# Performance work log

Measured on AMD Instinct MI355X. Metric: run time of the kernel, lower is better.

The kernel has to match this reference:

```python
import jax, jax.numpy as jnp
import numpy as np

B, N, D = 4, 2048, 512
H = 8
DH = D // H
FF = 2 * D


def setup_inputs() -> dict:
    key = jax.random.key(0)
    ks = jax.random.split(key, 16)
    s = lambda fan_in: 1.0 / np.sqrt(fan_in)
    inp = {
        "x0": jax.random.normal(ks[0], (B, N, D), jnp.float32),
        "x1": jax.random.normal(ks[1], (B, N, D), jnp.float32),
        # projections (torch Linear: weight [out, in])
        "Wqk": jax.random.uniform(ks[2], (D, D), jnp.float32, -s(D), s(D)),
        "bqk": jax.random.uniform(ks[3], (D,), jnp.float32, -s(D), s(D)),
        "Wv": jax.random.uniform(ks[4], (D, D), jnp.float32, -s(D), s(D)),
        "bv": jax.random.uniform(ks[5], (D,), jnp.float32, -s(D), s(D)),
        "Wo": jax.random.uniform(ks[6], (D, D), jnp.float32, -s(D), s(D)),
        "bo": jax.random.uniform(ks[7], (D,), jnp.float32, -s(D), s(D)),
        # FFN: Linear(2D,2D) -> LayerNorm(2D) -> GELU -> Linear(2D,D)
        "Wf1": jax.random.uniform(ks[8], (FF, FF), jnp.float32, -s(FF), s(FF)),
        "bf1": jax.random.uniform(ks[9], (FF,), jnp.float32, -s(FF), s(FF)),
        "ln_g": jnp.ones((FF,), jnp.float32),
        "ln_b": jnp.zeros((FF,), jnp.float32),
        "Wf2": jax.random.uniform(ks[10], (D, FF), jnp.float32, -s(FF), s(FF)),
        "bf2": jax.random.uniform(ks[11], (D,), jnp.float32, -s(FF), s(FF)),
    }
    return inp


def _split_heads(t):
    # [B,N,D] -> [B,H,N,DH]
    return t.reshape(B, N, H, DH).transpose(0, 2, 1, 3)


def _attn(q, k, v):
    # q,k,v: [B,H,N,DH]; scale by sqrt(d_k) as in the torch Attention module
    scores = jnp.einsum("bhnd,bhmd->bhnm", q, k) / jnp.sqrt(jnp.float32(DH))
    attn = jax.nn.softmax(scores, axis=-1)
    return jnp.einsum("bhnm,bhmd->bhnd", attn, v)


def _merge_heads(t):
    # [B,H,N,DH] -> [B,N,D]
    return t.transpose(0, 2, 1, 3).reshape(B, N, D)


def _ffn(x, Wf1, bf1, ln_g, ln_b, Wf2, bf2):
    h = x @ Wf1.T + bf1
    mu = jnp.mean(h, axis=-1, keepdims=True)
    var = jnp.mean(jnp.square(h - mu), axis=-1, keepdims=True)
    h = (h - mu) / jnp.sqrt(var + 1e-5) * ln_g + ln_b
    h = jax.nn.gelu(h, approximate=False)
    return h @ Wf2.T + bf2


def reference(x0, x1, Wqk, bqk, Wv, bv, Wo, bo, Wf1, bf1, ln_g, ln_b, Wf2, bf2):
    qk0 = _split_heads(x0 @ Wqk.T + bqk)
    qk1 = _split_heads(x1 @ Wqk.T + bqk)
    v0 = _split_heads(x0 @ Wv.T + bv)
    v1 = _split_heads(x1 @ Wv.T + bv)

    m0 = _merge_heads(_attn(qk0, qk1, v1)) @ Wo.T + bo
    m1 = _merge_heads(_attn(qk1, qk0, v0)) @ Wo.T + bo

    y0 = x0 + _ffn(jnp.concatenate([x0, m0], -1), Wf1, bf1, ln_g, ln_b, Wf2, bf2)
    y1 = x1 + _ffn(jnp.concatenate([x1, m1], -1), Wf1, bf1, ln_g, ln_b, Wf2, bf2)
    return (y0, y1)
```

## Files before the change

kernel.cpp:

```cpp
#include <hip/hip_runtime.h>
#include <hip/hip_bf16.h>
#include <math.h>

typedef __bf16 bf16;
typedef __bf16 bf16x8 __attribute__((ext_vector_type(8)));
typedef __bf16 bf16x4 __attribute__((ext_vector_type(4)));
typedef float  f32x4  __attribute__((ext_vector_type(4)));
typedef float  f32x16 __attribute__((ext_vector_type(16)));
typedef unsigned int u32x2 __attribute__((ext_vector_type(2)));

#define DEVI __device__ __forceinline__

DEVI void async16(bf16* lds, const bf16* g) {
    __builtin_amdgcn_global_load_lds(
        (const __attribute__((address_space(1))) unsigned int*)g,
        (__attribute__((address_space(3))) unsigned int*)lds, 16, 0, 0);
}
DEVI f32x4 mfma16(bf16x8 a, bf16x8 b, f32x4 c) {
    return __builtin_amdgcn_mfma_f32_16x16x32_bf16(a, b, c, 0, 0, 0);
}
DEVI f32x16 mfma32(bf16x8 a, bf16x8 b, f32x16 c) {
    return __builtin_amdgcn_mfma_f32_32x32x16_bf16(a, b, c, 0, 0, 0);
}
DEVI unsigned cvtpk(float lo, float hi) {
    unsigned r;
    asm("v_cvt_pk_bf16_f32 %0, %1, %2" : "=v"(r) : "v"(lo), "v"(hi));
    return r;
}
DEVI void pl32(unsigned &a, unsigned &b) {
    u32x2 r = __builtin_amdgcn_permlane32_swap(a, b, false, false);
    a = r.x; b = r.y;
}
DEVI bf16x8 mk8(unsigned a0, unsigned a1, unsigned b0, unsigned b1) {
    union { unsigned u[4]; bf16x8 v; } U;
    U.u[0] = a0; U.u[1] = a1; U.u[2] = b0; U.u[3] = b1;
    return U.v;
}

__global__ __launch_bounds__(256) void prep(
    const float* __restrict__ x0, const float* __restrict__ x1, bf16* __restrict__ Xbf,
    const float* __restrict__ Wqk, const float* __restrict__ Wv,
    const float* __restrict__ Wf1, const float* __restrict__ Wf2,
    bf16* __restrict__ Wqkv, bf16* __restrict__ Wbig, bf16* __restrict__ Wf1Rb,
    bf16* __restrict__ Wf2b,
    const float* __restrict__ Wo, bf16* __restrict__ WoT,
    const float* __restrict__ bo, const float* __restrict__ bf1,
    float* __restrict__ bf1p)
{
    __shared__ float Ls[64][65];
    const int bid = blockIdx.x, t = threadIdx.x;
    if (bid < 8192) {
        long i = (long)bid * 256 + t;
        long r = i >> 7, c = (i & 127) * 4;
        const float* src = (r < 8192) ? (x0 + r * 512 + c) : (x1 + (r - 8192) * 512 + c);
        float4 v = *(const float4*)src;
        bf16x4 o;
        o[0] = (bf16)v.x; o[1] = (bf16)v.y; o[2] = (bf16)v.z; o[3] = (bf16)v.w;
        *(bf16x4*)(Xbf + r * 1024 + c) = o;
    } else if (bid < 10240) {
        long i = (long)(bid - 8192) * 256 + t;
        const float* s; bf16* d;
        if (i < 131072) {
            s = (i < 65536) ? Wqk + i * 4 : Wv + (i - 65536) * 4;
            d = Wqkv + i * 4;
        } else if (i < 393216) {
            long e = (i - 131072) * 4, r = e >> 10, c = e & 1023;
            s = Wf1 + e;
            d = (c < 512) ? (Wbig + r * 1024 + c) : (Wf1Rb + r * 512 + (c - 512));
        } else {
            s = Wf2 + (i - 393216) * 4;
            d = Wf2b + (i - 393216) * 4;
        }
        float4 v = *(const float4*)s;
        bf16x4 o;
        o[0] = (bf16)v.x; o[1] = (bf16)v.y; o[2] = (bf16)v.z; o[3] = (bf16)v.w;
        *(bf16x4*)d = o;
    } else if (bid < 10304) {
        const int bb = bid - 10240;
        const int bi = bb & 7, bj = bb >> 3;
        const int i0 = bi * 64, j0 = bj * 64;
        const int r0 = t >> 4, c4 = (t & 15) * 4;
#pragma unroll
        for (int it = 0; it < 4; it++) {
            int row = r0 + 16 * it;
            float4 v = *(const float4*)(Wo + (long)(i0 + row) * 512 + j0 + c4);
            Ls[row][c4] = v.x; Ls[row][c4 + 1] = v.y;
            Ls[row][c4 + 2] = v.z; Ls[row][c4 + 3] = v.w;
        }
        __syncthreads();
#pragma unroll
        for (int it = 0; it < 4; it++) {
            int orow = r0 + 16 * it;
            bf16x4 o;
#pragma unroll
            for (int k = 0; k < 4; k++) o[k] = (bf16)Ls[c4 + k][orow];
            *(bf16x4*)(WoT + (long)(j0 + orow) * 512 + i0 + c4) = o;
        }
    } else {
        const int w = t >> 6, lane = t & 63;
        const int row = (bid - 10304) * 4 + w;
        const float* rp = Wf1 + (long)row * 1024 + 512 + lane * 8;
        float4 a = *(const float4*)rp;
        float4 b = *(const float4*)(rp + 4);
        const float* bp = bo + lane * 8;
        float4 c = *(const float4*)bp;
        float4 d = *(const float4*)(bp + 4);
        float s = a.x * c.x + a.y * c.y + a.z * c.z + a.w * c.w +
                  b.x * d.x + b.y * d.y + b.z * d.z + b.w * d.w;
#pragma unroll
        for (int k = 1; k < 64; k <<= 1) s += __shfl_xor(s, k);
        if (lane == 0) bf1p[row] = bf1[row] + s;
    }
}

template <int MODE>
__global__ __launch_bounds__(256) void gemm_bt(
    const bf16* __restrict__ A, long lda,
    const bf16* __restrict__ B, long ldb,
    const float* __restrict__ bias,
    void* __restrict__ Cout, long ldc,
    const float* __restrict__ res0, const float* __restrict__ res1,
    const float* __restrict__ bias2, void* __restrict__ Cout2,
    int M, int N, int K, float scale)
{
    __shared__ bf16 As[128 * 64];
    __shared__ bf16 Bs[128 * 64];
    const int t = threadIdx.x;
    const int w = t >> 6, lane = t & 63, quad = lane >> 4, m15 = lane & 15;
    const int wm = w >> 1, wn = w & 1;
    const int nbx = N >> 7;
    const int xcd = blockIdx.x & 7, local = blockIdx.x >> 3;
    const int mtiles_per_xcd = (int)(gridDim.x >> 3) / nbx;
    const int by = xcd * mtiles_per_xcd + local / nbx;
    const int bx = local % nbx;
    const long m0 = (long)by * 128, n0 = (long)bx * 128;

    f32x4 acc[4][4] = {};

    for (int k0 = 0; k0 < K; k0 += 64) {
#pragma unroll
        for (int i = 0; i < 4; i++) {
            int idx = i * 256 + t, row = idx >> 3, p = idx & 7;
            int gc = k0 + ((p ^ (row & 7)) * 8);
            async16(As + idx * 8, A + (m0 + row) * lda + gc);
            async16(Bs + idx * 8, B + (n0 + row) * ldb + gc);
        }
        __syncthreads();
#pragma unroll
        for (int kk = 0; kk < 2; kk++) {
            bf16x8 af[4], bfr[4];
#pragma unroll
            for (int mt = 0; mt < 4; mt++) {
                int row = wm * 64 + mt * 16 + m15;
                af[mt] = *(const bf16x8*)(As + row * 64 + (((kk * 4 + quad) ^ (row & 7)) * 8));
            }
#pragma unroll
            for (int nt = 0; nt < 4; nt++) {
                int row = wn * 64 + nt * 16 + m15;
                bfr[nt] = *(const bf16x8*)(Bs + row * 64 + (((kk * 4 + quad) ^ (row & 7)) * 8));
            }
#pragma unroll
            for (int mt = 0; mt < 4; mt++)
#pragma unroll
                for (int nt = 0; nt < 4; nt++)
                    acc[mt][nt] = mfma16(af[mt], bfr[nt], acc[mt][nt]);
        }
        __syncthreads();
    }

#pragma unroll
    for (int nt = 0; nt < 4; nt++) {
        long col = n0 + wn * 64 + nt * 16 + m15;
#pragma unroll
        for (int mt = 0; mt < 4; mt++) {
            long row = m0 + wm * 64 + mt * 16 + quad * 4;
            if (MODE == 0) {
                bf16* C = (bf16*)Cout;
                float bs = bias[col];
#pragma unroll
                for (int r = 0; r < 4; r++)
                    C[(row + r) * ldc + col] = (bf16)(acc[mt][nt][r] + bs);
            } else if (MODE == 4) {
                bf16* C = (bf16*)Cout;
#pragma unroll
                for (int r = 0; r < 4; r++)
                    C[(row + r) * ldc + col] = (bf16)acc[mt][nt][r];
            } else {
                float* C = (float*)Cout;
                float bs = bias[col];
#pragma unroll
                for (int r = 0; r < 4; r++) {
                    long grow = row + r;
                    const float* rs = (grow < 8192) ? (res0 + grow * 512)
                                                    : (res1 + (grow - 8192) * 512);
                    C[grow * ldc + col] = acc[mt][nt][r] + bs + rs[col];
                }
            }
        }
    }
}

template <int MODE>
__global__ __launch_bounds__(512, 2) void pipe_gemm(
    const bf16* __restrict__ A, long lda,
    const bf16* __restrict__ B, long ldb,
    const float* __restrict__ bias,
    void* __restrict__ Cout, long ldc,
    const float* __restrict__ bias2, void* __restrict__ Cout2,
    int M, int N, int K, float scale)
{
    __shared__ bf16 lds[65536];
    bf16* As = lds;
    bf16* Bs = lds + 32768;

    const int t = threadIdx.x;
    const int w = t >> 6, lane = t & 63, quad = lane >> 4, m15 = lane & 15;
    const int wm = w >> 2, wn = w & 3;
    const int nbx = N >> 8;
    const int xcd = blockIdx.x & 7, local = blockIdx.x >> 3;
    const int mtiles_per_xcd = (int)(gridDim.x >> 3) / nbx;
    const int by = xcd * mtiles_per_xcd + local / nbx;
    const int bx = local % nbx;
    const long m0 = (long)by * 256, n0 = (long)bx * 256;
    const int nt = K >> 6;

    f32x4 acc[8][4] = {};

    auto stage = [&](int kt) {
        const int slot = kt & 1;
        bf16* Ad = As + slot * 16384;
        bf16* Bd = Bs + slot * 16384;
        const int k0 = kt * 64;
#pragma unroll
        for (int i = 0; i < 4; i++) {
            int idx = i * 512 + t, row = idx >> 3, p = idx & 7;
            int gc = k0 + ((p ^ (row & 7)) * 8);
            async16(Ad + idx * 8, A + (m0 + row) * lda + gc);
        }
#pragma unroll
        for (int i = 0; i < 4; i++) {
            int idx = i * 512 + t, row = idx >> 3, p = idx & 7;
            int gc = k0 + ((p ^ (row & 7)) * 8);
            async16(Bd + idx * 8, B + (n0 + row) * ldb + gc);
        }
    };

    stage(0);
    stage(1);

    for (int kt = 0; kt < nt; kt++) {
        if (kt + 1 < nt) {
            asm volatile("s_waitcnt vmcnt(8)" ::: "memory");
        } else {
            asm volatile("s_waitcnt vmcnt(0)" ::: "memory");
        }
        __builtin_amdgcn_s_barrier();
        __builtin_amdgcn_sched_barrier(0);

        const bf16* Asl = As + (kt & 1) * 16384;
        const bf16* Bsl = Bs + (kt & 1) * 16384;
#pragma unroll
        for (int ksub = 0; ksub < 2; ksub++) {
            bf16x8 af[8], bfr[4];
#pragma unroll
            for (int mf = 0; mf < 8; mf++) {
                int row = wm * 128 + mf * 16 + m15;
                af[mf] = *(const bf16x8*)(Asl + row * 64 + (((ksub * 4 + quad) ^ (row & 7)) * 8));
            }
#pragma unroll
            for (int nf = 0; nf < 4; nf++) {
                int row = wn * 64 + nf * 16 + m15;
                bfr[nf] = *(const bf16x8*)(Bsl + row * 64 + (((ksub * 4 + quad) ^ (row & 7)) * 8));
            }
            __builtin_amdgcn_s_setprio(1);
#pragma unroll
            for (int mf = 0; mf < 8; mf++)
#pragma unroll
                for (int nf = 0; nf < 4; nf++)
                    acc[mf][nf] = mfma16(af[mf], bfr[nf], acc[mf][nf]);
            __builtin_amdgcn_s_setprio(0);
        }

        __builtin_amdgcn_sched_barrier(0);
        __builtin_amdgcn_s_barrier();
        __builtin_amdgcn_sched_barrier(0);
        if (kt + 2 < nt) stage(kt + 2);
    }

#pragma unroll
    for (int nf = 0; nf < 4; nf++) {
        long col = n0 + wn * 64 + nf * 16 + m15;
#pragma unroll
        for (int mf = 0; mf < 8; mf++) {
            long row = m0 + wm * 128 + mf * 16 + quad * 4;
            if (MODE == 0) {
                bf16* C = (bf16*)Cout;
                float bs = bias[col];
#pragma unroll
                for (int r = 0; r < 4; r++)
                    C[(row + r) * ldc + col] = (bf16)(acc[mf][nf][r] + bs);
            } else {
                if (col < 512) {
                    bf16* C = (bf16*)Cout;
                    float bs = bias[col];
#pragma unroll
                    for (int r = 0; r < 4; r++)
                        C[(row + r) * ldc + col] = (bf16)((acc[mf][nf][r] + bs) * scale);
                } else {
                    bf16* V = (bf16*)Cout2;
                    long v = col - 512;
                    float bs = bias2[v];
                    bf16x4 pv;
#pragma unroll
                    for (int r = 0; r < 4; r++) pv[r] = (bf16)(acc[mf][nf][r] + bs);
                    *(bf16x4*)(V + v * 16384 + row) = pv;
                }
            }
        }
    }
}

__global__ __launch_bounds__(256, 4) void flash_attn(const bf16* __restrict__ QK,
                                                     const bf16* __restrict__ VT,
                                                     bf16* __restrict__ o)
{
    __shared__ bf16 lds[16384];

    const int t = threadIdx.x, w = t >> 6, lane = t & 63;
    const int l31 = lane & 31, hi = lane >> 5;
    const int j = blockIdx.x;
    const int hs = j & 63;
    const int qt = j >> 6;
    const int h = hs & 7, b = (hs >> 3) & 3, dir = hs >> 5;
    const long qrow0  = (long)dir * 8192 + b * 2048 + qt * 128;
    const long kvrow0 = (long)(1 - dir) * 8192 + b * 2048;
    const int hc = h * 64;

#pragma unroll
    for (int i = 0; i < 4; i++) {
        int idx = i * 256 + t, row = idx >> 3, p = idx & 7;
        async16(lds + idx * 8, QK + (qrow0 + row) * 512 + hc + ((p ^ (row & 7)) * 8));
    }
    __syncthreads();
    bf16x8 qf[4];
    {
        int qrow = w * 32 + l31;
#pragma unroll
        for (int kd = 0; kd < 4; kd++)
            qf[kd] = *(const bf16x8*)(lds + qrow * 64 + (((kd * 2 + hi) ^ (qrow & 7)) * 8));
    }
    __syncthreads();

#pragma unroll
    for (int i = 0; i < 2; i++) {
        int idx = i * 256 + t, row = idx >> 3, p = idx & 7;
        async16(lds + idx * 8, QK + (kvrow0 + row) * 512 + hc + ((p ^ (row & 7)) * 8));
    }
#pragma unroll
    for (int i = 0; i < 2; i++) {
        int idx = i * 256 + t, row = idx >> 3, p = idx & 7;
        async16(lds + 8192 + idx * 8, VT + (long)(hc + row) * 16384 + kvrow0 + ((p ^ (row & 7)) * 8));
    }

    f32x16 oacc[2] = {};
    f32x16 racc = {};
    bf16x8 ones;
#pragma unroll
    for (int k = 0; k < 8; k++) ones[k] = (bf16)1.0f;

    for (int kb = 0; kb < 32; kb++) {
        bf16* Kc = lds + (kb & 1) * 4096;
        bf16* Vc = lds + 8192 + (kb & 1) * 4096;

        asm volatile("s_waitcnt vmcnt(0)" ::: "memory");
        __builtin_amdgcn_s_barrier();

        if (kb < 31) {
            const long knext = kvrow0 + (kb + 1) * 64;
            bf16* Kn = lds + ((kb + 1) & 1) * 4096;
            bf16* Vn = lds + 8192 + ((kb + 1) & 1) * 4096;
#pragma unroll
            for (int i = 0; i < 2; i++) {
                int idx = i * 256 + t, row = idx >> 3, p = idx & 7;
                async16(Kn + idx * 8, QK + (knext + row) * 512 + hc + ((p ^ (row & 7)) * 8));
            }
#pragma unroll
            for (int i = 0; i < 2; i++) {
                int idx = i * 256 + t, row = idx >> 3, p = idx & 7;
                async16(Vn + idx * 8, VT + (long)(hc + row) * 16384 + knext + ((p ^ (row & 7)) * 8));
            }
        }

#pragma unroll
        for (int kb2 = 0; kb2 < 2; kb2++) {
            const int krow = kb2 * 32 + l31;
            const int ksw = krow & 7;
            bf16x8 kf0 = *(const bf16x8*)(Kc + krow * 64 + (((0 + hi) ^ ksw) * 8));
            bf16x8 kf1 = *(const bf16x8*)(Kc + krow * 64 + (((2 + hi) ^ ksw) * 8));
            bf16x8 kf2 = *(const bf16x8*)(Kc + krow * 64 + (((4 + hi) ^ ksw) * 8));
            bf16x8 kf3 = *(const bf16x8*)(Kc + krow * 64 + (((6 + hi) ^ ksw) * 8));

            f32x16 s0 = {};
            __builtin_amdgcn_s_setprio(1);
            s0 = mfma32(kf0, qf[0], s0);
            s0 = mfma32(kf1, qf[1], s0);
            s0 = mfma32(kf2, qf[2], s0);
            s0 = mfma32(kf3, qf[3], s0);
            __builtin_amdgcn_s_setprio(0);

#pragma unroll
            for (int r = 0; r < 16; r++) s0[r] = exp2f(s0[r]);

#pragma unroll
            for (int sh = 0; sh < 2; sh++) {
                const int ks = kb2 * 2 + sh;
                unsigned a00 = cvtpk(s0[8 * sh + 0], s0[8 * sh + 1]);
                unsigned a01 = cvtpk(s0[8 * sh + 2], s0[8 * sh + 3]);
                unsigned b00 = cvtpk(s0[8 * sh + 4], s0[8 * sh + 5]);
                unsigned b01 = cvtpk(s0[8 * sh + 6], s0[8 * sh + 7]);
                pl32(a00, b00); pl32(a01, b01);
                bf16x8 pa0 = mk8(a00, a01, b00, b01);

                __builtin_amdgcn_s_setprio(1);
#pragma unroll
                for (int db = 0; db < 2; db++) {
                    const int vrow = db * 32 + l31;
                    bf16x8 vf = *(const bf16x8*)(Vc + vrow * 64 + (((ks * 2 + hi) ^ (vrow & 7)) * 8));
                    oacc[db] = mfma32(pa0, vf, oacc[db]);
                }
                racc = mfma32(pa0, ones, racc);
                __builtin_amdgcn_s_setprio(0);
            }
        }
    }

#pragma unroll
    for (int reg = 0; reg < 16; reg++) {
        const int q = (reg & 3) + 8 * (reg >> 2) + 4 * hi;
        const float inv = 1.f / racc[reg];
        const long row = qrow0 + w * 32 + q;
#pragma unroll
        for (int db = 0; db < 2; db++)
            o[row * 1024 + hc + db * 32 + l31] = (bf16)(oacc[db][reg] * inv);
    }
}

__global__ __launch_bounds__(256) void ln_gelu(bf16* __restrict__ H,
                                               const float* __restrict__ g,
                                               const float* __restrict__ bta)
{
    const int row = blockIdx.x, t = threadIdx.x;
    const int w = t >> 6, lane = t & 63;
    bf16* hp = H + (long)row * 1024 + t * 4;
    bf16x4 hv = *(const bf16x4*)hp;
    float h[4];
#pragma unroll
    for (int j = 0; j < 4; j++) h[j] = (float)hv[j];
    float s1 = h[0] + h[1] + h[2] + h[3];
    float s2 = h[0] * h[0] + h[1] * h[1] + h[2] * h[2] + h[3] * h[3];
#pragma unroll
    for (int d = 1; d < 64; d <<= 1) {
        s1 += __shfl_xor(s1, d);
        s2 += __shfl_xor(s2, d);
    }
    __shared__ float rbuf[8];
    if (lane == 0) { rbuf[w] = s1; rbuf[4 + w] = s2; }
    __syncthreads();
    s1 = rbuf[0] + rbuf[1] + rbuf[2] + rbuf[3];
    s2 = rbuf[4] + rbuf[5] + rbuf[6] + rbuf[7];
    const float mu = s1 * (1.f / 1024.f);
    const float var = s2 * (1.f / 1024.f) - mu * mu;
    const float rstd = rsqrtf(var + 1e-5f);
    bf16x4 out;
#pragma unroll
    for (int j = 0; j < 4; j++) {
        int c = t * 4 + j;
        float x = (h[j] - mu) * rstd * g[c] + bta[c];
        float y = 0.5f * x * (1.f + erff(x * 0.70710678118654752f));
        out[j] = (bf16)y;
    }
    *(bf16x4*)hp = out;
}

extern "C" void kernel_launch(void* const* d_in, const int* in_sizes, int n_in,
                              void* d_out, int out_size, void* d_ws, size_t ws_size,
                              hipStream_t stream)
{
    const float* x0  = (const float*)d_in[0];
    const float* x1  = (const float*)d_in[1];
    const float* Wqk = (const float*)d_in[2];
    const float* bqk = (const float*)d_in[3];
    const float* Wv  = (const float*)d_in[4];
    const float* bv  = (const float*)d_in[5];
    const float* Wo  = (const float*)d_in[6];
    const float* bo  = (const float*)d_in[7];
    const float* Wf1 = (const float*)d_in[8];
    const float* bf1 = (const float*)d_in[9];
    const float* lng = (const float*)d_in[10];
    const float* lnb = (const float*)d_in[11];
    const float* Wf2 = (const float*)d_in[12];
    const float* bf2 = (const float*)d_in[13];

    char* ws = (char*)d_ws;
    bf16* Xbf   = (bf16*)ws; ws += 16384L * 1024 * 2;
    bf16* QKbf  = (bf16*)ws;
    bf16* Hbuf  = (bf16*)ws;
    ws += 16384L * 512 * 2;
    bf16* VtG   = (bf16*)ws; ws += 16384L * 512 * 2;
    bf16* Wqkv  = (bf16*)ws; ws += 1024L * 512 * 2;
    bf16* Wbig  = (bf16*)ws; ws += 1024L * 1024 * 2;
    bf16* Wf1Rb = (bf16*)ws; ws += 1024L * 512 * 2;
    bf16* Wf2b  = (bf16*)ws; ws += 512L * 1024 * 2;
    bf16* WoT   = (bf16*)ws; ws += 512L * 512 * 2;
    float* bf1p = (float*)ws; ws += 1024 * 4;

    const float qs = 0.42466090014400953f;

    prep<<<10560, 256, 0, stream>>>(x0, x1, Xbf, Wqk, Wv, Wf1, Wf2,
                                    Wqkv, Wbig, Wf1Rb, Wf2b, Wo, WoT, bo, bf1, bf1p);

    gemm_bt<4><<<32, 256, 0, stream>>>(Wf1Rb, 512, WoT, 512, nullptr,
                                       Wbig + 512, 1024, nullptr, nullptr,
                                       nullptr, nullptr, 1024, 512, 512, 1.f);

    pipe_gemm<5><<<256, 512, 0, stream>>>(Xbf, 1024, Wqkv, 512, bqk,
                                          QKbf, 512, bv, VtG,
                                          16384, 1024, 512, qs);

    flash_attn<<<1024, 256, 0, stream>>>(QKbf, VtG, Xbf + 512);

    pipe_gemm<0><<<256, 512, 0, stream>>>(Xbf, 1024, Wbig, 1024, bf1p,
                                          Hbuf, 1024, nullptr, nullptr,
                                          16384, 1024, 1024, 1.f);
    ln_gelu<<<16384, 256, 0, stream>>>(Hbuf, lng, lnb);
    gemm_bt<1><<<512, 256, 0, stream>>>(Hbuf, 1024, Wf2b, 1024, bf2,
                                        d_out, 512, x0, x1,
                                        nullptr, nullptr, 16384, 512, 1024, 1.f);
}
```

Measured before the change: 353.3 us.

## Software-pipeline attention softmax/PV across key blocks and add pipelined FFN2 GEMM

The flash attention loop is restructured so the second half's softmax and PV step for one key block runs during the next block's QK MFMAs. V gets a triple-buffered LDS ring so the previous block's V stays valid while the next one loads. The final FFN projection moves from gemm_bt to a new 512-thread double-buffered GEMM with XCD-aware tile mapping and fused bias and residual. This adds LDS use and register pressure (an extra score accumulator) in exchange for better MFMA/VALU overlap.

Result: slower. 360.7 us (+2.1%).

```diff
diff --git a/kernel.cpp b/kernel.cpp
--- a/kernel.cpp
+++ b/kernel.cpp
@@ -320,11 +320,117 @@
     }
 }
 
+__global__ __launch_bounds__(512, 2) void pipe_ffn2(
+    const bf16* __restrict__ A, long lda,
+    const bf16* __restrict__ B, long ldb,
+    const float* __restrict__ bias,
+    float* __restrict__ C, long ldc,
+    const float* __restrict__ res0, const float* __restrict__ res1,
+    int M, int N, int K)
+{
+    __shared__ bf16 lds[49152];
+    bf16* As = lds;
+    bf16* Bs = lds + 16384;
+
+    const int t = threadIdx.x;
+    const int w = t >> 6, lane = t & 63, quad = lane >> 4, m15 = lane & 15;
+    const int wm = w >> 2, wn = w & 3;
+    const int nbx = N >> 8;
+    const int xcd = blockIdx.x & 7, local = blockIdx.x >> 3;
+    const int mtiles_per_xcd = (int)(gridDim.x >> 3) / nbx;
+    const int by = xcd * mtiles_per_xcd + local / nbx;
+    const int bx = local % nbx;
+    const long m0 = (long)by * 128, n0 = (long)bx * 256;
+    const int nt = K >> 6;
+
+    f32x4 acc[4][4] = {};
+
+    auto stage = [&](int kt) {
+        const int slot = kt & 1;
+        bf16* Ad = As + slot * 8192;
+        bf16* Bd = Bs + slot * 16384;
+        const int k0 = kt * 64;
+#pragma unroll
+        for (int i = 0; i < 2; i++) {
+            int idx = i * 512 + t, row = idx >> 3, p = idx & 7;
+            int gc = k0 + ((p ^ (row & 7)) * 8);
+            async16(Ad + idx * 8, A + (m0 + row) * lda + gc);
+        }
+#pragma unroll
+        for (int i = 0; i < 4; i++) {
+            int idx = i * 512 + t, row = idx >> 3, p = idx & 7;
+            int gc = k0 + ((p ^ (row & 7)) * 8);
+            async16(Bd + idx * 8, B + (n0 + row) * ldb + gc);
+        }
+    };
+
+    stage(0);
+    stage(1);
+
+    for (int kt = 0; kt < nt; kt++) {
+        if (kt + 1 < nt) {
+            asm volatile("s_waitcnt vmcnt(6)" ::: "memory");
+        } else {
+            asm volatile("s_waitcnt vmcnt(0)" ::: "memory");
+        }
+        __builtin_amdgcn_s_barrier();
+        __builtin_amdgcn_sched_barrier(0);
+
+        const bf16* Asl = As + (kt & 1) * 8192;
+        const bf16* Bsl = Bs + (kt & 1) * 16384;
+#pragma unroll
+        for (int ksub = 0; ksub < 2; ksub++) {
+            bf16x8 af[4], bfr[4];
+#pragma unroll
+            for (int mf = 0; mf < 4; mf++) {
+                int row = wm * 64 + mf * 16 + m15;
+                af[mf] = *(const bf16x8*)(Asl + row * 64 + (((ksub * 4 + quad) ^ (row & 7)) * 8));
+            }
+#pragma unroll
+            for (int nf = 0; nf < 4; nf++) {
+                int row = wn * 64 + nf * 16 + m15;
+                bfr[nf] = *(const bf16x8*)(Bsl + row * 64 + (((ksub * 4 + quad) ^ (row & 7)) * 8));
+            }
+            __builtin_amdgcn_s_setprio(1);
+#pragma unroll
+            for (int mf = 0; mf < 4; mf++)
+#pragma unroll
+                for (int nf = 0; nf < 4; nf++)
+                    acc[mf][nf] = mfma16(af[mf], bfr[nf], acc[mf][nf]);
+            __builtin_amdgcn_s_setprio(0);
+        }
+
+        __builtin_amdgcn_sched_barrier(0);
+        __builtin_amdgcn_s_barrier();
+        __builtin_amdgcn_sched_barrier(0);
+        if (kt + 2 < nt) stage(kt + 2);
+    }
+
+#pragma unroll
+    for (int nf = 0; nf < 4; nf++) {
+        long col = n0 + wn * 64 + nf * 16 + m15;
+        float bs = bias[col];
+#pragma unroll
+        for (int mf = 0; mf < 4; mf++) {
+            long row = m0 + wm * 64 + mf * 16 + quad * 4;
+#pragma unroll
+            for (int r = 0; r < 4; r++) {
+                long grow = row + r;
+                const float* rs = (grow < 8192) ? (res0 + grow * 512)
+                                                : (res1 + (grow - 8192) * 512);
+                C[grow * ldc + col] = acc[mf][nf][r] + bs + rs[col];
+            }
+        }
+    }
+}
+
 __global__ __launch_bounds__(256, 4) void flash_attn(const bf16* __restrict__ QK,
                                                      const bf16* __restrict__ VT,
                                                      bf16* __restrict__ o)
 {
-    __shared__ bf16 lds[16384];
+    __shared__ bf16 lds[20480];
+    bf16* Ks = lds;
+    bf16* Vs = lds + 8192;
 
     const int t = threadIdx.x, w = t >> 6, lane = t & 63;
     const int l31 = lane & 31, hi = lane >> 5;
@@ -354,31 +460,57 @@
 #pragma unroll
     for (int i = 0; i < 2; i++) {
         int idx = i * 256 + t, row = idx >> 3, p = idx & 7;
-        async16(lds + idx * 8, QK + (kvrow0 + row) * 512 + hc + ((p ^ (row & 7)) * 8));
+        async16(Ks + idx * 8, QK + (kvrow0 + row) * 512 + hc + ((p ^ (row & 7)) * 8));
     }
 #pragma unroll
     for (int i = 0; i < 2; i++) {
         int idx = i * 256 + t, row = idx >> 3, p = idx & 7;
-        async16(lds + 8192 + idx * 8, VT + (long)(hc + row) * 16384 + kvrow0 + ((p ^ (row & 7)) * 8));
+        async16(Vs + idx * 8, VT + (long)(hc + row) * 16384 + kvrow0 + ((p ^ (row & 7)) * 8));
     }
 
     f32x16 oacc[2] = {};
     f32x16 racc = {};
+    f32x16 sP = {};
     bf16x8 ones;
 #pragma unroll
-    for (int k = 0; k < 8; k++) ones[k] = (bf16)1.0f;
+    for (int k2 = 0; k2 < 8; k2++) ones[k2] = (bf16)1.0f;
+
+    auto SM_PV = [&](f32x16 &s, const bf16* Vb, int ksbase) {
+#pragma unroll
+        for (int r = 0; r < 16; r++) s[r] = exp2f(s[r]);
+#pragma unroll
+        for (int sh = 0; sh < 2; sh++) {
+            unsigned a0 = cvtpk(s[8 * sh + 0], s[8 * sh + 1]);
+            unsigned a1 = cvtpk(s[8 * sh + 2], s[8 * sh + 3]);
+            unsigned b0 = cvtpk(s[8 * sh + 4], s[8 * sh + 5]);
+            unsigned b1 = cvtpk(s[8 * sh + 6], s[8 * sh + 7]);
+            pl32(a0, b0); pl32(a1, b1);
+            bf16x8 pa = mk8(a0, a1, b0, b1);
+            const int ks = ksbase + sh;
+            __builtin_amdgcn_s_setprio(1);
+#pragma unroll
+            for (int db = 0; db < 2; db++) {
+                const int vrow = db * 32 + l31;
+                bf16x8 vf = *(const bf16x8*)(Vb + vrow * 64 + (((ks * 2 + hi) ^ (vrow & 7)) * 8));
+                oacc[db] = mfma32(pa, vf, oacc[db]);
+            }
+            racc = mfma32(pa, ones, racc);
+            __builtin_amdgcn_s_setprio(0);
+        }
+    };
 
     for (int kb = 0; kb < 32; kb++) {
-        bf16* Kc = lds + (kb & 1) * 4096;
-        bf16* Vc = lds + 8192 + (kb & 1) * 4096;
+        bf16* Kc = Ks + (kb & 1) * 4096;
+        bf16* Vc = Vs + (kb % 3) * 4096;
+        const bf16* Vp = Vs + ((kb + 2) % 3) * 4096;
 
         asm volatile("s_waitcnt vmcnt(0)" ::: "memory");
         __builtin_amdgcn_s_barrier();
 
         if (kb < 31) {
             const long knext = kvrow0 + (kb + 1) * 64;
-            bf16* Kn = lds + ((kb + 1) & 1) * 4096;
-            bf16* Vn = lds + 8192 + ((kb + 1) & 1) * 4096;
+            bf16* Kn = Ks + ((kb + 1) & 1) * 4096;
+            bf16* Vn = Vs + ((kb + 1) % 3) * 4096;
 #pragma unroll
             for (int i = 0; i < 2; i++) {
                 int idx = i * 256 + t, row = idx >> 3, p = idx & 7;
@@ -391,48 +523,45 @@
             }
         }
 
-#pragma unroll
-        for (int kb2 = 0; kb2 < 2; kb2++) {
-            const int krow = kb2 * 32 + l31;
+        f32x16 sA = {};
+        {
+            const int krow = l31;
             const int ksw = krow & 7;
             bf16x8 kf0 = *(const bf16x8*)(Kc + krow * 64 + (((0 + hi) ^ ksw) * 8));
             bf16x8 kf1 = *(const bf16x8*)(Kc + krow * 64 + (((2 + hi) ^ ksw) * 8));
             bf16x8 kf2 = *(const bf16x8*)(Kc + krow * 64 + (((4 + hi) ^ ksw) * 8));
             bf16x8 kf3 = *(const bf16x8*)(Kc + krow * 64 + (((6 + hi) ^ ksw) * 8));
-
-            f32x16 s0 = {};
             __builtin_amdgcn_s_setprio(1);
-            s0 = mfma32(kf0, qf[0], s0);
-            s0 = mfma32(kf1, qf[1], s0);
-            s0 = mfma32(kf2, qf[2], s0);
-            s0 = mfma32(kf3, qf[3], s0);
+            sA = mfma32(kf0, qf[0], sA);
+            sA = mfma32(kf1, qf[1], sA);
+            sA = mfma32(kf2, qf[2], sA);
+            sA = mfma32(kf3, qf[3], sA);
             __builtin_amdgcn_s_setprio(0);
-
-#pragma unroll
-            for (int r = 0; r < 16; r++) s0[r] = exp2f(s0[r]);
-
-#pragma unroll
-            for (int sh = 0; sh < 2; sh++) {
-                const int ks = kb2 * 2 + sh;
-                unsigned a00 = cvtpk(s0[8 * sh + 0], s0[8 * sh + 1]);
-                unsigned a01 = cvtpk(s0[8 * sh + 2], s0[8 * sh + 3]);
-                unsigned b00 = cvtpk(s0[8 * sh + 4], s0[8 * sh + 5]);
-                unsigned b01 = cvtpk(s0[8 * sh + 6], s0[8 * sh + 7]);
-                pl32(a00, b00); pl32(a01, b01);
-                bf16x8 pa0 = mk8(a00, a01, b00, b01);
-
-                __builtin_amdgcn_s_setprio(1);
-#pragma unroll
-                for (int db = 0; db < 2; db++) {
-                    const int vrow = db * 32 + l31;
-                    bf16x8 vf = *(const bf16x8*)(Vc + vrow * 64 + (((ks * 2 + hi) ^ (vrow & 7)) * 8));
-                    oacc[db] = mfma32(pa0, vf, oacc[db]);
-                }
-                racc = mfma32(pa0, ones, racc);
-                __builtin_amdgcn_s_setprio(0);
-            }
-        }
-    }
+        }
+
+        if (kb > 0) SM_PV(sP, Vp, 2);
+
+        f32x16 sB = {};
+        {
+            const int krow = 32 + l31;
+            const int ksw = krow & 7;
+            bf16x8 kf0 = *(const bf16x8*)(Kc + krow * 64 + (((0 + hi) ^ ksw) * 8));
+            bf16x8 kf1 = *(const bf16x8*)(Kc + krow * 64 + (((2 + hi) ^ ksw) * 8));
+            bf16x8 kf2 = *(const bf16x8*)(Kc + krow * 64 + (((4 + hi) ^ ksw) * 8));
+            bf16x8 kf3 = *(const bf16x8*)(Kc + krow * 64 + (((6 + hi) ^ ksw) * 8));
+            __builtin_amdgcn_s_setprio(1);
+            sB = mfma32(kf0, qf[0], sB);
+            sB = mfma32(kf1, qf[1], sB);
+            sB = mfma32(kf2, qf[2], sB);
+            sB = mfma32(kf3, qf[3], sB);
+            __builtin_amdgcn_s_setprio(0);
+        }
+
+        SM_PV(sA, Vc, 0);
+
+        sP = sB;
+    }
+    SM_PV(sP, Vs + 4096, 2);
 
 #pragma unroll
     for (int reg = 0; reg < 16; reg++) {
@@ -533,7 +662,7 @@
                                           Hbuf, 1024, nullptr, nullptr,
                                           16384, 1024, 1024, 1.f);
     ln_gelu<<<16384, 256, 0, stream>>>(Hbuf, lng, lnb);
-    gemm_bt<1><<<512, 256, 0, stream>>>(Hbuf, 1024, Wf2b, 1024, bf2,
-                                        d_out, 512, x0, x1,
-                                        nullptr, nullptr, 16384, 512, 1024, 1.f);
-}
+    pipe_ffn2<<<256, 512, 0, stream>>>(Hbuf, 1024, Wf2b, 1024, bf2,
+                                       (float*)d_out, 512, x0, x1,
+                                       16384, 512, 1024);
+}
```
